# Kernel tuning notes

Measured on AMD Instinct MI355X. Metric: run time of the kernel, lower is better.

Reference implementation:

```python
import jax, jax.numpy as jnp
import numpy as np

N, K, M = 4096, 128, 512  # conformers, dihedrals, atoms


def setup_inputs() -> dict:
    key = jax.random.key(0)
    k1, k2 = jax.random.split(key)
    inp = jax.random.normal(k1, (N, K), dtype=jnp.float32)          # target dihedral deltas (rad)
    pos0 = jax.random.normal(k2, (N, M, 3), dtype=jnp.float32)      # initial conformer coordinates
    base = jnp.arange(K, dtype=jnp.int32)
    # chain molecule: dihedral k defined by atoms (k, k+1, k+2, k+3)
    angles = jnp.stack([base, base + 1, base + 2, base + 3], axis=1)  # (K, 4)
    # rdkit toBeMovedIdxList on a chain for bond (k+1, k+2): atoms k+3 .. M-1 move
    move_mask = jnp.arange(M)[None, :] > (base + 2)[:, None]          # (K, M) bool
    return {"input": inp, "pos0": pos0, "angles": angles, "move_mask": move_mask}


def _rot_matrix(theta, axis):
    # rdkit Transform3D::SetRotation: R = (1-cos)*aa^T + [[c,-sZ,sY],[sZ,c,-sX],[-sY,sX,c]]
    cosT = jnp.cos(theta)
    sinT = jnp.sin(theta)
    t = 1.0 - cosT
    outer = t[:, None, None] * axis[:, :, None] * axis[:, None, :]   # (N,3,3)
    X, Y, Z = axis[:, 0], axis[:, 1], axis[:, 2]
    mat1 = jnp.stack(
        [cosT, -sinT * Z, sinT * Y,
         sinT * Z, cosT, -sinT * X,
         -sinT * Y, sinT * X, cosT], axis=1
    ).reshape(-1, 3, 3)
    return outer + mat1


def _step(pos, x):
    ang, mask, theta = x                       # (4,), (M,), (N,)
    p = jnp.take(pos, ang, axis=1)             # (N,4,3) gather of i,j,k,l atoms
    rIJ = p[:, 1] - p[:, 0]
    rJK = p[:, 2] - p[:, 1]
    rKL = p[:, 3] - p[:, 2]
    nIJK = jnp.cross(rIJ, rJK)
    nJKL = jnp.cross(rJK, rKL)
    m = jnp.cross(nIJK, rJK)
    nrm = lambda v: jnp.linalg.norm(v, axis=-1)
    sin_arg = jnp.sum(m * nJKL, axis=-1) / (nrm(nJKL) * nrm(m))
    cos_arg = jnp.sum(nIJK * nJKL, axis=-1) / (nrm(nIJK) * nrm(nJKL))
    values = theta + jnp.arctan2(sin_arg, cos_arg)   # rotation angle per conformer
    begin = p[:, 1]                                   # rotation axis origin (atom j)
    d = p[:, 2] - p[:, 1]
    # torch.nn.functional.normalize with eps=1e-12
    axis = d / jnp.maximum(jnp.linalg.norm(d, axis=-1, keepdims=True), 1e-12)
    R = _rot_matrix(values, axis)                     # (N,3,3)
    rotated = jnp.einsum('nij,nmj->nmi', R, pos - begin[:, None, :]) + begin[:, None, :]
    pos = jnp.where(mask[None, :, None], rotated, pos)
    return pos, None


def reference(input, pos0, angles, move_mask):
    xs = (angles, move_mask, input.T)                 # scan over K dihedrals (sequential recurrence)
    pos, _ = jax.lax.scan(_step, pos0, xs)
    return pos
```

## Files before the change

kernel.cpp:

```cpp
#include <hip/hip_runtime.h>


#define NK 128
#define NM 512
#define NMOL 4096
#define TPB 256
#define MPW 4

struct Aff { float qw, qx, qy, qz, tx, ty, tz; };

__device__ __forceinline__ void qrot(float qw, float qx, float qy, float qz,
                                     float vx, float vy, float vz,
                                     float& ox, float& oy, float& oz) {
    const float ux = qy*vz - qz*vy + qw*vx;
    const float uy = qz*vx - qx*vz + qw*vy;
    const float uz = qx*vy - qy*vx + qw*vz;
    ox = vx + 2.f*(qy*uz - qz*uy);
    oy = vy + 2.f*(qz*ux - qx*uz);
    oz = vz + 2.f*(qx*uy - qy*ux);
}

__device__ __forceinline__ Aff aff_compose(const Aff& Q, const Aff& P) {
    Aff r;
    r.qw = Q.qw*P.qw - Q.qx*P.qx - Q.qy*P.qy - Q.qz*P.qz;
    r.qx = Q.qw*P.qx + Q.qx*P.qw + Q.qy*P.qz - Q.qz*P.qy;
    r.qy = Q.qw*P.qy - Q.qx*P.qz + Q.qy*P.qw + Q.qz*P.qx;
    r.qz = Q.qw*P.qz + Q.qx*P.qy - Q.qy*P.qx + Q.qz*P.qw;
    float rx, ry, rz;
    qrot(Q.qw, Q.qx, Q.qy, Q.qz, P.tx, P.ty, P.tz, rx, ry, rz);
    r.tx = rx + Q.tx; r.ty = ry + Q.ty; r.tz = rz + Q.tz;
    return r;
}

__device__ __forceinline__ void qnorm(Aff& a) {
    const float r = rsqrtf(a.qw*a.qw + a.qx*a.qx + a.qy*a.qy + a.qz*a.qz);
    a.qw *= r; a.qx *= r; a.qy *= r; a.qz *= r;
}

__device__ __forceinline__ Aff make_step(float c, float s,
                                         float ax, float ay, float az,
                                         float px, float py, float pz) {
    const float hc = sqrtf(fmaxf(0.f, 0.5f*(1.f + c)));
    const float hs = copysignf(sqrtf(fmaxf(0.f, 0.5f*(1.f - c))), s);
    Aff b; b.qw = hc; b.qx = hs*ax; b.qy = hs*ay; b.qz = hs*az;
    float rx, ry, rz;
    qrot(b.qw, b.qx, b.qy, b.qz, px, py, pz, rx, ry, rz);
    b.tx = px - rx; b.ty = py - ry; b.tz = pz - rz;
    return b;
}

#define SHFL_AFF_UP(D, S, off)                                           \
    D.qw = __shfl_up(S.qw, off, 64); D.qx = __shfl_up(S.qx, off, 64);    \
    D.qy = __shfl_up(S.qy, off, 64); D.qz = __shfl_up(S.qz, off, 64);    \
    D.tx = __shfl_up(S.tx, off, 64); D.ty = __shfl_up(S.ty, off, 64);    \
    D.tz = __shfl_up(S.tz, off, 64);

__global__ __launch_bounds__(TPB, 4) void dihedral_fused_kernel(
    const float* __restrict__ theta,
    const float* __restrict__ pos0,
    float* __restrict__ out)
{
    const int tid  = threadIdx.x;
    const int lane = tid & 63;
    const int wid  = tid >> 6;
    const int mol  = blockIdx.x * MPW + wid;
    const float4* __restrict__ pb4 = (const float4*)(pos0 + (size_t)mol * (NM*3));
    float4*       __restrict__ ob4 = (float4*)(out  + (size_t)mol * (NM*3));

    __shared__ float sA[MPW][400];
    __shared__ float sO[MPW][400];

    float4 h0 = pb4[lane];
    float4 h1; if (lane < 35) h1 = pb4[64 + lane];
    const float2 th2 = ((const float2*)(theta + (size_t)mol * NK))[lane];
    float4 Ta0, Ta1, Ta2, Tb0, Tb1, Tb2;
    { const int b = 99 + 3*lane; Ta0 = pb4[b]; Ta1 = pb4[b+1]; Ta2 = pb4[b+2]; }
    const bool hasB = (lane < 31);
    if (hasB) { const int b = 99 + 3*(64 + lane); Tb0 = pb4[b]; Tb1 = pb4[b+1]; Tb2 = pb4[b+2]; }

    float4* sA4 = (float4*)sA[wid];
    sA4[lane] = h0;
    if (lane < 35) sA4[64 + lane] = h1;

    float A[16];
    const float2* ap2 = (const float2*)&sA[wid][lane * 6];
    #pragma unroll
    for (int i = 0; i < 7; ++i) { const float2 v = ap2[i]; A[2*i] = v.x; A[2*i+1] = v.y; }
    A[14] = sA[wid][lane * 6 + 14];

    const float v01x=A[3]-A[0],  v01y=A[4]-A[1],   v01z=A[5]-A[2];
    const float v12x=A[6]-A[3],  v12y=A[7]-A[4],   v12z=A[8]-A[5];
    const float v23x=A[9]-A[6],  v23y=A[10]-A[7],  v23z=A[11]-A[8];
    const float v34x=A[12]-A[9], v34y=A[13]-A[10], v34z=A[14]-A[11];
    const float n1x=v01y*v12z-v01z*v12y, n1y=v01z*v12x-v01x*v12z, n1z=v01x*v12y-v01y*v12x;
    const float n2x=v12y*v23z-v12z*v23y, n2y=v12z*v23x-v12x*v23z, n2z=v12x*v23y-v12y*v23x;
    const float n3x=v23y*v34z-v23z*v34y, n3y=v23z*v34x-v23x*v34z, n3z=v23x*v34y-v23y*v34x;
    const float mex=n1y*v12z-n1z*v12y,  mey=n1z*v12x-n1x*v12z,  mez=n1x*v12y-n1y*v12x;
    const float mox=n2y*v23z-n2z*v23y,  moy=n2z*v23x-n2x*v23z,  moz=n2x*v23y-n2y*v23x;
    const float L1=n1x*n1x+n1y*n1y+n1z*n1z;
    const float L2=n2x*n2x+n2y*n2y+n2z*n2z;
    const float L3=n3x*n3x+n3y*n3y+n3z*n3z;
    const float Lme=mex*mex+mey*mey+mez*mez;
    const float Lmo=mox*mox+moy*moy+moz*moz;

    float sphE = (mex*n2x+mey*n2y+mez*n2z) * rsqrtf(Lme*L2);
    float cphE = (n1x*n2x+n1y*n2y+n1z*n2z) * rsqrtf(L1*L2);
    { const float rn = rsqrtf(sphE*sphE + cphE*cphE); sphE *= rn; cphE *= rn; }
    float sthE, cthE; sincosf(th2.x, &sthE, &cthE);
    const float cE = cthE*cphE - sthE*sphE;
    const float sE = sthE*cphE + cthE*sphE;
    const float LjkE = v12x*v12x+v12y*v12y+v12z*v12z;
    const float invE = rsqrtf(fmaxf(LjkE, 1e-24f));
    Aff Bev = make_step(cE, sE, v12x*invE, v12y*invE, v12z*invE, A[3], A[4], A[5]);

    float sphO = (mox*n3x+moy*n3y+moz*n3z) * rsqrtf(Lmo*L3);
    float cphO = (n2x*n3x+n2y*n3y+n2z*n3z) * rsqrtf(L2*L3);
    { const float rn = rsqrtf(sphO*sphO + cphO*cphO); sphO *= rn; cphO *= rn; }
    float sthO, cthO; sincosf(th2.y, &sthO, &cthO);
    const float cO = cthO*cphO - sthO*sphO;
    const float sO_ = sthO*cphO + cthO*sphO;
    const float LjkO = v23x*v23x+v23y*v23y+v23z*v23z;
    const float invO = rsqrtf(fmaxf(LjkO, 1e-24f));
    Aff Bod = make_step(cO, sO_, v23x*invO, v23y*invO, v23z*invO, A[6], A[7], A[8]);

    Aff S = aff_compose(Bev, Bod);

    #pragma unroll
    for (int off = 1; off < 64; off <<= 1) {
        Aff Q; SHFL_AFF_UP(Q, S, off);
        if (lane >= off) S = aff_compose(Q, S);
    }
    Aff E; SHFL_AFF_UP(E, S, 1);
    if (lane == 0) { E.qw = 1.f; E.qx = E.qy = E.qz = 0.f; E.tx = E.ty = E.tz = 0.f; }
    Aff Pe = aff_compose(E, Bev);
    qnorm(Pe); qnorm(S);

    {
        float ox, oy, oz;
        float* op = &sO[wid][lane * 6 + 9];
        qrot(Pe.qw, Pe.qx, Pe.qy, Pe.qz, A[9], A[10], A[11], ox, oy, oz);
        op[0] = ox + Pe.tx; op[1] = oy + Pe.ty; op[2] = oz + Pe.tz;
        qrot(S.qw, S.qx, S.qy, S.qz, A[12], A[13], A[14], ox, oy, oz);
        op[3] = ox + S.tx;  op[4] = oy + S.ty;  op[5] = oz + S.tz;
    }
    if (lane < 9) sO[wid][lane] = sA[wid][lane];
    if (lane == 63) {
        float ox, oy, oz;
        qrot(S.qw, S.qx, S.qy, S.qz, sA[wid][393], sA[wid][394], sA[wid][395], ox, oy, oz);
        sO[wid][393] = ox + S.tx; sO[wid][394] = oy + S.ty; sO[wid][395] = oz + S.tz;
    }

    Aff F;
    F.qw = __shfl(S.qw, 63, 64); F.qx = __shfl(S.qx, 63, 64);
    F.qy = __shfl(S.qy, 63, 64); F.qz = __shfl(S.qz, 63, 64);
    F.tx = __shfl(S.tx, 63, 64); F.ty = __shfl(S.ty, 63, 64);
    F.tz = __shfl(S.tz, 63, 64);
    const float f00 = 1.f - 2.f*(F.qy*F.qy + F.qz*F.qz);
    const float f01 = 2.f*(F.qx*F.qy - F.qw*F.qz);
    const float f02 = 2.f*(F.qx*F.qz + F.qw*F.qy);
    const float f10 = 2.f*(F.qx*F.qy + F.qw*F.qz);
    const float f11 = 1.f - 2.f*(F.qx*F.qx + F.qz*F.qz);
    const float f12 = 2.f*(F.qy*F.qz - F.qw*F.qx);
    const float f20 = 2.f*(F.qx*F.qz - F.qw*F.qy);
    const float f21 = 2.f*(F.qy*F.qz + F.qw*F.qx);
    const float f22 = 1.f - 2.f*(F.qx*F.qx + F.qy*F.qy);

    const float4* sO4 = (const float4*)sO[wid];
    ob4[lane] = sO4[lane];
    if (lane < 35) ob4[64 + lane] = sO4[64 + lane];

    #define TAIL_EMIT(b, va, vb, vc)                                          \
    do {                                                                      \
        const float x0=va.x, y0=va.y, z0=va.z;                                \
        const float x1=va.w, y1=vb.x, z1=vb.y;                                \
        const float x2=vb.z, y2=vb.w, z2=vc.x;                                \
        const float x3=vc.y, y3=vc.z, z3=vc.w;                                \
        float4 o0, o1, o2;                                                    \
        o0.x = f00*x0+f01*y0+f02*z0+F.tx; o0.y = f10*x0+f11*y0+f12*z0+F.ty;   \
        o0.z = f20*x0+f21*y0+f22*z0+F.tz; o0.w = f00*x1+f01*y1+f02*z1+F.tx;   \
        o1.x = f10*x1+f11*y1+f12*z1+F.ty; o1.y = f20*x1+f21*y1+f22*z1+F.tz;   \
        o1.z = f00*x2+f01*y2+f02*z2+F.tx; o1.w = f10*x2+f11*y2+f12*z2+F.ty;   \
        o2.x = f20*x2+f21*y2+f22*z2+F.tz; o2.y = f00*x3+f01*y3+f02*z3+F.tx;   \
        o2.z = f10*x3+f11*y3+f12*z3+F.ty; o2.w = f20*x3+f21*y3+f22*z3+F.tz;   \
        ob4[(b)] = o0; ob4[(b)+1] = o1; ob4[(b)+2] = o2;                      \
    } while (0)

    TAIL_EMIT(99 + 3*lane, Ta0, Ta1, Ta2);
    if (hasB) TAIL_EMIT(99 + 3*(64 + lane), Tb0, Tb1, Tb2);
    #undef TAIL_EMIT
}

extern "C" void kernel_launch(void* const* d_in, const int* in_sizes, int n_in,
                              void* d_out, int out_size, void* d_ws, size_t ws_size,
                              hipStream_t stream) {
    const float* theta = (const float*)d_in[0];
    const float* pos0  = (const float*)d_in[1];
    float* out = (float*)d_out;
    dihedral_fused_kernel<<<NMOL / MPW, TPB, 0, stream>>>(theta, pos0, out);
}
```

Before: 19.01 us.

## Split each molecule across a 3-wave block: one scan wave, two tail-transform waves

```diff
diff --git a/kernel.cpp b/kernel.cpp
--- a/kernel.cpp
+++ b/kernel.cpp
@@ -4,8 +4,7 @@
 #define NK 128
 #define NM 512
 #define NMOL 4096
-#define TPB 256
-#define MPW 4
+#define TPB 192
 
 struct Aff { float qw, qx, qy, qz, tx, ty, tz; };
 
@@ -55,7 +54,7 @@
     D.tx = __shfl_up(S.tx, off, 64); D.ty = __shfl_up(S.ty, off, 64);    \
     D.tz = __shfl_up(S.tz, off, 64);
 
-__global__ __launch_bounds__(TPB, 4) void dihedral_fused_kernel(
+__global__ __launch_bounds__(TPB, 8) void dihedral_block_kernel(
     const float* __restrict__ theta,
     const float* __restrict__ pos0,
     float* __restrict__ out)
@@ -63,131 +62,132 @@
     const int tid  = threadIdx.x;
     const int lane = tid & 63;
     const int wid  = tid >> 6;
-    const int mol  = blockIdx.x * MPW + wid;
+    const int mol  = blockIdx.x;
     const float4* __restrict__ pb4 = (const float4*)(pos0 + (size_t)mol * (NM*3));
     float4*       __restrict__ ob4 = (float4*)(out  + (size_t)mol * (NM*3));
 
-    __shared__ float sA[MPW][400];
-    __shared__ float sO[MPW][400];
-
-    float4 h0 = pb4[lane];
-    float4 h1; if (lane < 35) h1 = pb4[64 + lane];
-    const float2 th2 = ((const float2*)(theta + (size_t)mol * NK))[lane];
-    float4 Ta0, Ta1, Ta2, Tb0, Tb1, Tb2;
-    { const int b = 99 + 3*lane; Ta0 = pb4[b]; Ta1 = pb4[b+1]; Ta2 = pb4[b+2]; }
-    const bool hasB = (lane < 31);
-    if (hasB) { const int b = 99 + 3*(64 + lane); Tb0 = pb4[b]; Tb1 = pb4[b+1]; Tb2 = pb4[b+2]; }
-
-    float4* sA4 = (float4*)sA[wid];
-    sA4[lane] = h0;
-    if (lane < 35) sA4[64 + lane] = h1;
-
-    float A[16];
-    const float2* ap2 = (const float2*)&sA[wid][lane * 6];
-    #pragma unroll
-    for (int i = 0; i < 7; ++i) { const float2 v = ap2[i]; A[2*i] = v.x; A[2*i+1] = v.y; }
-    A[14] = sA[wid][lane * 6 + 14];
-
-    const float v01x=A[3]-A[0],  v01y=A[4]-A[1],   v01z=A[5]-A[2];
-    const float v12x=A[6]-A[3],  v12y=A[7]-A[4],   v12z=A[8]-A[5];
-    const float v23x=A[9]-A[6],  v23y=A[10]-A[7],  v23z=A[11]-A[8];
-    const float v34x=A[12]-A[9], v34y=A[13]-A[10], v34z=A[14]-A[11];
-    const float n1x=v01y*v12z-v01z*v12y, n1y=v01z*v12x-v01x*v12z, n1z=v01x*v12y-v01y*v12x;
-    const float n2x=v12y*v23z-v12z*v23y, n2y=v12z*v23x-v12x*v23z, n2z=v12x*v23y-v12y*v23x;
-    const float n3x=v23y*v34z-v23z*v34y, n3y=v23z*v34x-v23x*v34z, n3z=v23x*v34y-v23y*v34x;
-    const float mex=n1y*v12z-n1z*v12y,  mey=n1z*v12x-n1x*v12z,  mez=n1x*v12y-n1y*v12x;
-    const float mox=n2y*v23z-n2z*v23y,  moy=n2z*v23x-n2x*v23z,  moz=n2x*v23y-n2y*v23x;
-    const float L1=n1x*n1x+n1y*n1y+n1z*n1z;
-    const float L2=n2x*n2x+n2y*n2y+n2z*n2z;
-    const float L3=n3x*n3x+n3y*n3y+n3z*n3z;
-    const float Lme=mex*mex+mey*mey+mez*mez;
-    const float Lmo=mox*mox+moy*moy+moz*moz;
-
-    float sphE = (mex*n2x+mey*n2y+mez*n2z) * rsqrtf(Lme*L2);
-    float cphE = (n1x*n2x+n1y*n2y+n1z*n2z) * rsqrtf(L1*L2);
-    { const float rn = rsqrtf(sphE*sphE + cphE*cphE); sphE *= rn; cphE *= rn; }
-    float sthE, cthE; sincosf(th2.x, &sthE, &cthE);
-    const float cE = cthE*cphE - sthE*sphE;
-    const float sE = sthE*cphE + cthE*sphE;
-    const float LjkE = v12x*v12x+v12y*v12y+v12z*v12z;
-    const float invE = rsqrtf(fmaxf(LjkE, 1e-24f));
-    Aff Bev = make_step(cE, sE, v12x*invE, v12y*invE, v12z*invE, A[3], A[4], A[5]);
-
-    float sphO = (mox*n3x+moy*n3y+moz*n3z) * rsqrtf(Lmo*L3);
-    float cphO = (n2x*n3x+n2y*n3y+n2z*n3z) * rsqrtf(L2*L3);
-    { const float rn = rsqrtf(sphO*sphO + cphO*cphO); sphO *= rn; cphO *= rn; }
-    float sthO, cthO; sincosf(th2.y, &sthO, &cthO);
-    const float cO = cthO*cphO - sthO*sphO;
-    const float sO_ = sthO*cphO + cthO*sphO;
-    const float LjkO = v23x*v23x+v23y*v23y+v23z*v23z;
-    const float invO = rsqrtf(fmaxf(LjkO, 1e-24f));
-    Aff Bod = make_step(cO, sO_, v23x*invO, v23y*invO, v23z*invO, A[6], A[7], A[8]);
-
-    Aff S = aff_compose(Bev, Bod);
-
-    #pragma unroll
-    for (int off = 1; off < 64; off <<= 1) {
-        Aff Q; SHFL_AFF_UP(Q, S, off);
-        if (lane >= off) S = aff_compose(Q, S);
+    __shared__ float sA[400];
+    __shared__ float sO[400];
+    __shared__ float sF[12];
+
+    const int t = tid - 64;
+    const bool isTail = (wid > 0) && (t < 95);
+    float4 T0, T1, T2;
+    if (isTail) { const int b = 99 + 3*t; T0 = pb4[b]; T1 = pb4[b+1]; T2 = pb4[b+2]; }
+
+    if (wid == 0) {
+        float4* sA4 = (float4*)sA;
+        float4 h0 = pb4[lane];
+        float4 h1; if (lane < 35) h1 = pb4[64 + lane];
+        const float2 th2 = ((const float2*)(theta + (size_t)mol * NK))[lane];
+        sA4[lane] = h0;
+        if (lane < 35) sA4[64 + lane] = h1;
+
+        float A[16];
+        const float2* ap2 = (const float2*)&sA[lane * 6];
+        #pragma unroll
+        for (int i = 0; i < 7; ++i) { const float2 v = ap2[i]; A[2*i] = v.x; A[2*i+1] = v.y; }
+        A[14] = sA[lane * 6 + 14];
+
+        const float v01x=A[3]-A[0],  v01y=A[4]-A[1],   v01z=A[5]-A[2];
+        const float v12x=A[6]-A[3],  v12y=A[7]-A[4],   v12z=A[8]-A[5];
+        const float v23x=A[9]-A[6],  v23y=A[10]-A[7],  v23z=A[11]-A[8];
+        const float v34x=A[12]-A[9], v34y=A[13]-A[10], v34z=A[14]-A[11];
+        const float n1x=v01y*v12z-v01z*v12y, n1y=v01z*v12x-v01x*v12z, n1z=v01x*v12y-v01y*v12x;
+        const float n2x=v12y*v23z-v12z*v23y, n2y=v12z*v23x-v12x*v23z, n2z=v12x*v23y-v12y*v23x;
+        const float n3x=v23y*v34z-v23z*v34y, n3y=v23z*v34x-v23x*v34z, n3z=v23x*v34y-v23y*v34x;
+        const float mex=n1y*v12z-n1z*v12y,  mey=n1z*v12x-n1x*v12z,  mez=n1x*v12y-n1y*v12x;
+        const float mox=n2y*v23z-n2z*v23y,  moy=n2z*v23x-n2x*v23z,  moz=n2x*v23y-n2y*v23x;
+        const float L1=n1x*n1x+n1y*n1y+n1z*n1z;
+        const float L2=n2x*n2x+n2y*n2y+n2z*n2z;
+        const float L3=n3x*n3x+n3y*n3y+n3z*n3z;
+        const float Lme=mex*mex+mey*mey+mez*mez;
+        const float Lmo=mox*mox+moy*moy+moz*moz;
+
+        float sphE = (mex*n2x+mey*n2y+mez*n2z) * rsqrtf(Lme*L2);
+        float cphE = (n1x*n2x+n1y*n2y+n1z*n2z) * rsqrtf(L1*L2);
+        { const float rn = rsqrtf(sphE*sphE + cphE*cphE); sphE *= rn; cphE *= rn; }
+        float sthE, cthE; sincosf(th2.x, &sthE, &cthE);
+        const float cE = cthE*cphE - sthE*sphE;
+        const float sE = sthE*cphE + cthE*sphE;
+        const float LjkE = v12x*v12x+v12y*v12y+v12z*v12z;
+        const float invE = rsqrtf(fmaxf(LjkE, 1e-24f));
+        Aff Bev = make_step(cE, sE, v12x*invE, v12y*invE, v12z*invE, A[3], A[4], A[5]);
+
+        float sphO = (mox*n3x+moy*n3y+moz*n3z) * rsqrtf(Lmo*L3);
+        float cphO = (n2x*n3x+n2y*n3y+n2z*n3z) * rsqrtf(L2*L3);
+        { const float rn = rsqrtf(sphO*sphO + cphO*cphO); sphO *= rn; cphO *= rn; }
+        float sthO, cthO; sincosf(th2.y, &sthO, &cthO);
+        const float cO = cthO*cphO - sthO*sphO;
+        const float sO_ = sthO*cphO + cthO*sphO;
+        const float LjkO = v23x*v23x+v23y*v23y+v23z*v23z;
+        const float invO = rsqrtf(fmaxf(LjkO, 1e-24f));
+        Aff Bod = make_step(cO, sO_, v23x*invO, v23y*invO, v23z*invO, A[6], A[7], A[8]);
+
+        Aff S = aff_compose(Bev, Bod);
+
+        #pragma unroll
+        for (int off = 1; off < 64; off <<= 1) {
+            Aff Q; SHFL_AFF_UP(Q, S, off);
+            if (lane >= off) S = aff_compose(Q, S);
+        }
+        Aff E; SHFL_AFF_UP(E, S, 1);
+        if (lane == 0) { E.qw = 1.f; E.qx = E.qy = E.qz = 0.f; E.tx = E.ty = E.tz = 0.f; }
+        Aff Pe = aff_compose(E, Bev);
+        qnorm(Pe); qnorm(S);
+
+        {
+            float ox, oy, oz;
+            float* op = &sO[lane * 6 + 9];
+            qrot(Pe.qw, Pe.qx, Pe.qy, Pe.qz, A[9], A[10], A[11], ox, oy, oz);
+            op[0] = ox + Pe.tx; op[1] = oy + Pe.ty; op[2] = oz + Pe.tz;
+            qrot(S.qw, S.qx, S.qy, S.qz, A[12], A[13], A[14], ox, oy, oz);
+            op[3] = ox + S.tx;  op[4] = oy + S.ty;  op[5] = oz + S.tz;
+        }
+        if (lane < 9) sO[lane] = sA[lane];
+        if (lane == 63) {
+            float ox, oy, oz;
+            qrot(S.qw, S.qx, S.qy, S.qz, sA[393], sA[394], sA[395], ox, oy, oz);
+            sO[393] = ox + S.tx; sO[394] = oy + S.ty; sO[395] = oz + S.tz;
+            const float qw=S.qw, qx=S.qx, qy=S.qy, qz=S.qz;
+            sF[0] = 1.f - 2.f*(qy*qy + qz*qz);
+            sF[1] = 2.f*(qx*qy - qw*qz);
+            sF[2] = 2.f*(qx*qz + qw*qy);
+            sF[3] = 2.f*(qx*qy + qw*qz);
+            sF[4] = 1.f - 2.f*(qx*qx + qz*qz);
+            sF[5] = 2.f*(qy*qz - qw*qx);
+            sF[6] = 2.f*(qx*qz - qw*qy);
+            sF[7] = 2.f*(qy*qz + qw*qx);
+            sF[8] = 1.f - 2.f*(qx*qx + qy*qy);
+            sF[9] = S.tx; sF[10] = S.ty; sF[11] = S.tz;
+        }
     }
-    Aff E; SHFL_AFF_UP(E, S, 1);
-    if (lane == 0) { E.qw = 1.f; E.qx = E.qy = E.qz = 0.f; E.tx = E.ty = E.tz = 0.f; }
-    Aff Pe = aff_compose(E, Bev);
-    qnorm(Pe); qnorm(S);
-
-    {
-        float ox, oy, oz;
-        float* op = &sO[wid][lane * 6 + 9];
-        qrot(Pe.qw, Pe.qx, Pe.qy, Pe.qz, A[9], A[10], A[11], ox, oy, oz);
-        op[0] = ox + Pe.tx; op[1] = oy + Pe.ty; op[2] = oz + Pe.tz;
-        qrot(S.qw, S.qx, S.qy, S.qz, A[12], A[13], A[14], ox, oy, oz);
-        op[3] = ox + S.tx;  op[4] = oy + S.ty;  op[5] = oz + S.tz;
+
+    __syncthreads();
+
+    if (wid == 0) {
+        const float4* sO4 = (const float4*)sO;
+        ob4[lane] = sO4[lane];
+        if (lane < 35) ob4[64 + lane] = sO4[64 + lane];
+    } else if (isTail) {
+        const float f00=sF[0], f01=sF[1], f02=sF[2];
+        const float f10=sF[3], f11=sF[4], f12=sF[5];
+        const float f20=sF[6], f21=sF[7], f22=sF[8];
+        const float ftx=sF[9], fty=sF[10], ftz=sF[11];
+        const float x0=T0.x, y0=T0.y, z0=T0.z;
+        const float x1=T0.w, y1=T1.x, z1=T1.y;
+        const float x2=T1.z, y2=T1.w, z2=T2.x;
+        const float x3=T2.y, y3=T2.z, z3=T2.w;
+        float4 o0, o1, o2;
+        o0.x = f00*x0+f01*y0+f02*z0+ftx; o0.y = f10*x0+f11*y0+f12*z0+fty;
+        o0.z = f20*x0+f21*y0+f22*z0+ftz; o0.w = f00*x1+f01*y1+f02*z1+ftx;
+        o1.x = f10*x1+f11*y1+f12*z1+fty; o1.y = f20*x1+f21*y1+f22*z1+ftz;
+        o1.z = f00*x2+f01*y2+f02*z2+ftx; o1.w = f10*x2+f11*y2+f12*z2+fty;
+        o2.x = f20*x2+f21*y2+f22*z2+ftz; o2.y = f00*x3+f01*y3+f02*z3+ftx;
+        o2.z = f10*x3+f11*y3+f12*z3+fty; o2.w = f20*x3+f21*y3+f22*z3+ftz;
+        const int b = 99 + 3*t;
+        ob4[b] = o0; ob4[b+1] = o1; ob4[b+2] = o2;
     }
-    if (lane < 9) sO[wid][lane] = sA[wid][lane];
-    if (lane == 63) {
-        float ox, oy, oz;
-        qrot(S.qw, S.qx, S.qy, S.qz, sA[wid][393], sA[wid][394], sA[wid][395], ox, oy, oz);
-        sO[wid][393] = ox + S.tx; sO[wid][394] = oy + S.ty; sO[wid][395] = oz + S.tz;
-    }
-
-    Aff F;
-    F.qw = __shfl(S.qw, 63, 64); F.qx = __shfl(S.qx, 63, 64);
-    F.qy = __shfl(S.qy, 63, 64); F.qz = __shfl(S.qz, 63, 64);
-    F.tx = __shfl(S.tx, 63, 64); F.ty = __shfl(S.ty, 63, 64);
-    F.tz = __shfl(S.tz, 63, 64);
-    const float f00 = 1.f - 2.f*(F.qy*F.qy + F.qz*F.qz);
-    const float f01 = 2.f*(F.qx*F.qy - F.qw*F.qz);
-    const float f02 = 2.f*(F.qx*F.qz + F.qw*F.qy);
-    const float f10 = 2.f*(F.qx*F.qy + F.qw*F.qz);
-    const float f11 = 1.f - 2.f*(F.qx*F.qx + F.qz*F.qz);
-    const float f12 = 2.f*(F.qy*F.qz - F.qw*F.qx);
-    const float f20 = 2.f*(F.qx*F.qz - F.qw*F.qy);
-    const float f21 = 2.f*(F.qy*F.qz + F.qw*F.qx);
-    const float f22 = 1.f - 2.f*(F.qx*F.qx + F.qy*F.qy);
-
-    const float4* sO4 = (const float4*)sO[wid];
-    ob4[lane] = sO4[lane];
-    if (lane < 35) ob4[64 + lane] = sO4[64 + lane];
-
-    #define TAIL_EMIT(b, va, vb, vc)                                          \
-    do {                                                                      \
-        const float x0=va.x, y0=va.y, z0=va.z;                                \
-        const float x1=va.w, y1=vb.x, z1=vb.y;                                \
-        const float x2=vb.z, y2=vb.w, z2=vc.x;                                \
-        const float x3=vc.y, y3=vc.z, z3=vc.w;                                \
-        float4 o0, o1, o2;                                                    \
-        o0.x = f00*x0+f01*y0+f02*z0+F.tx; o0.y = f10*x0+f11*y0+f12*z0+F.ty;   \
-        o0.z = f20*x0+f21*y0+f22*z0+F.tz; o0.w = f00*x1+f01*y1+f02*z1+F.tx;   \
-        o1.x = f10*x1+f11*y1+f12*z1+F.ty; o1.y = f20*x1+f21*y1+f22*z1+F.tz;   \
-        o1.z = f00*x2+f01*y2+f02*z2+F.tx; o1.w = f10*x2+f11*y2+f12*z2+F.ty;   \
-        o2.x = f20*x2+f21*y2+f22*z2+F.tz; o2.y = f00*x3+f01*y3+f02*z3+F.tx;   \
-        o2.z = f10*x3+f11*y3+f12*z3+F.ty; o2.w = f20*x3+f21*y3+f22*z3+F.tz;   \
-        ob4[(b)] = o0; ob4[(b)+1] = o1; ob4[(b)+2] = o2;                      \
-    } while (0)
-
-    TAIL_EMIT(99 + 3*lane, Ta0, Ta1, Ta2);
-    if (hasB) TAIL_EMIT(99 + 3*(64 + lane), Tb0, Tb1, Tb2);
-    #undef TAIL_EMIT
 }
 
 extern "C" void kernel_launch(void* const* d_in, const int* in_sizes, int n_in,
@@ -196,5 +196,5 @@
     const float* theta = (const float*)d_in[0];
     const float* pos0  = (const float*)d_in[1];
     float* out = (float*)d_out;
-    dihedral_fused_kernel<<<NMOL / MPW, TPB, 0, stream>>>(theta, pos0, out);
-}
+    dihedral_block_kernel<<<NMOL, TPB, 0, stream>>>(theta, pos0, out);
+}
```

Result: slower. 28.52 us (+50.0%).
